# Optimization experiments

Measured on AMD Instinct MI355X. Metric: run time of the kernel, lower is better.

## Reference

```python
import jax, jax.numpy as jnp
import numpy as np

B, T, C, H, HD = 4, 2048, 1024, 16, 64

def setup_inputs() -> dict:
    key = jax.random.key(0)
    ks = jax.random.split(key, 9)
    s = 1.0 / np.sqrt(C)
    return {
        "x":  jax.random.normal(ks[0], (B, T, C), jnp.float32),
        "Wq": jax.random.normal(ks[1], (H, C, HD), jnp.float32) * s,
        "bq": jax.random.normal(ks[2], (H, HD), jnp.float32) * 0.02,
        "Wk": jax.random.normal(ks[3], (H, C, HD), jnp.float32) * s,
        "bk": jax.random.normal(ks[4], (H, HD), jnp.float32) * 0.02,
        "Wv": jax.random.normal(ks[5], (H, C, HD), jnp.float32) * s,
        "bv": jax.random.normal(ks[6], (H, HD), jnp.float32) * 0.02,
        "Wo": jax.random.normal(ks[7], (C, C), jnp.float32) * s,
        "bo": jax.random.normal(ks[8], (C,), jnp.float32) * 0.02,
    }

def reference(x, Wq, bq, Wk, bk, Wv, bv, Wo, bo):
    # Batched per-head linear projections: [B,T,C] x [H,C,D] -> [B,H,T,D]
    q = jnp.einsum('btc,hcd->bhtd', x, Wq) + bq[None, :, None, :]
    k = jnp.einsum('btc,hcd->bhtd', x, Wk) + bk[None, :, None, :]
    v = jnp.einsum('btc,hcd->bhtd', x, Wv) + bv[None, :, None, :]
    scale = 1.0 / jnp.sqrt(jnp.asarray(HD, q.dtype))
    scores = jnp.einsum('bhtd,bhsd->bhts', q, k) * scale  # [B,H,T,T]
    causal = jnp.tril(jnp.ones((T, T), dtype=bool))
    scores = jnp.where(causal[None, None, :, :], scores, -jnp.inf)
    attn = jax.nn.softmax(scores, axis=-1)
    out = jnp.einsum('bhts,bhsd->bhtd', attn, v)          # [B,H,T,D]
    concat = out.transpose(0, 2, 1, 3).reshape(B, T, C)   # concat heads
    return concat @ Wo + bo
```

## Files before the change

### kernel.cpp

```cpp
#include <hip/hip_runtime.h>
#include <stdint.h>

#define TSEQ 2048
#define NHEAD 16

typedef __attribute__((ext_vector_type(8))) short bf16x8;
typedef __attribute__((ext_vector_type(4))) short bf16x4;
typedef __attribute__((ext_vector_type(4))) float f32x4;

__device__ __forceinline__ unsigned short f2bf(float f) {
  union { float f; uint32_t u; } c;
  c.f = f;
  uint32_t u = c.u;
  u += 0x7fffu + ((u >> 16) & 1u);
  return (unsigned short)(u >> 16);
}

__device__ __forceinline__ float fexp2(float x) {
#if __has_builtin(__builtin_amdgcn_exp2f)
  return __builtin_amdgcn_exp2f(x);
#else
  return __builtin_exp2f(x);
#endif
}

using as3_void  = __attribute__((address_space(3))) void;
using as1_cvoid = const __attribute__((address_space(1))) void;

__device__ __forceinline__ void gld_lds16(const void* g, void* l) {
  __builtin_amdgcn_global_load_lds((as1_cvoid*)g, (as3_void*)l, 16, 0, 0);
}


__global__ void cast_x_kernel(const float4* __restrict__ x, unsigned short* __restrict__ xb) {
  int i = blockIdx.x * 256 + threadIdx.x;
  float4 v = x[i];
  int e = i * 4;
  int m = e >> 10, k = e & 1023;
  int ks = k ^ ((m & 7) << 3);
  ushort4 o;
  o.x = f2bf(v.x); o.y = f2bf(v.y); o.z = f2bf(v.z); o.w = f2bf(v.w);
  *(ushort4*)(xb + (size_t)m * 1024 + ks) = o;
}

__global__ void repack_wqkv(const float* __restrict__ Wq, const float* __restrict__ Wk,
                            const float* __restrict__ Wv, unsigned short* __restrict__ BT) {
  __shared__ unsigned short tile[64][72];
  const float* W = (blockIdx.z == 0) ? Wq : (blockIdx.z == 1) ? Wk : Wv;
  const int h = blockIdx.y;
  const int c0 = blockIdx.x * 64;
  const int t = threadIdx.x;
  const float* src = W + ((size_t)h * 1024 + c0) * 64;
#pragma unroll
  for (int p = 0; p < 16; ++p) {
    int idx = p * 256 + t;
    int cc = idx >> 6, d = idx & 63;
    tile[cc][d] = f2bf(src[(size_t)cc * 64 + d]);
  }
  __syncthreads();
  unsigned short* dst = BT + ((size_t)blockIdx.z * 1024 + (size_t)h * 64) * 1024 + c0;
#pragma unroll
  for (int p = 0; p < 16; ++p) {
    int idx = p * 256 + t;
    int d = idx >> 6, cc = idx & 63;
    dst[(size_t)d * 1024 + (cc ^ ((d & 7) << 3))] = tile[cc][d];
  }
}

__global__ void repack_wo(const float* __restrict__ Wo, unsigned short* __restrict__ WoT) {
  __shared__ unsigned short tile[64][72];
  const int k0 = blockIdx.x * 64;
  const int n0 = blockIdx.y * 64;
  const int t = threadIdx.x;
#pragma unroll
  for (int p = 0; p < 16; ++p) {
    int idx = p * 256 + t;
    int kk = idx >> 6, nn = idx & 63;
    tile[kk][nn] = f2bf(Wo[(size_t)(k0 + kk) * 1024 + n0 + nn]);
  }
  __syncthreads();
#pragma unroll
  for (int p = 0; p < 16; ++p) {
    int idx = p * 256 + t;
    int nn = idx >> 6, kk = idx & 63;
    WoT[(size_t)(n0 + nn) * 1024 + k0 + (kk ^ ((nn & 7) << 3))] = tile[kk][nn];
  }
}


template <int MODE>
__global__ __launch_bounds__(256) void gemm_bt(
    const unsigned short* __restrict__ A, const unsigned short* __restrict__ BTm,
    const float* __restrict__ bias0, const float* __restrict__ bias1,
    const float* __restrict__ bias2,
    unsigned short* __restrict__ qo, unsigned short* __restrict__ ko,
    unsigned short* __restrict__ vto, float* __restrict__ outf,
    int K, int N) {
  __shared__ __align__(16) char lds[65536];

  const int tid = threadIdx.x, lane = tid & 63, wv = tid >> 6;
  const int wr = wv >> 1, wc = wv & 1;
  const int g = lane >> 4, r = lane & 15;
  const int m0 = blockIdx.x * 128, n0 = blockIdx.y * 128;
  const int xr = (r & 7) << 4;

  f32x4 acc[4][4] = {};

  const int arow = tid >> 3;
  const int acol = (tid & 7) * 8;
  const unsigned short* Ab = A + (size_t)(m0 + arow) * K + acol;
  const unsigned short* Bb = BTm + (size_t)(n0 + arow) * K + acol;

#define GSTAGE(b, kel) do {                                                 \
    char* ab_ = lds + (b) * 32768 + wv * 1024;                              \
    _Pragma("unroll") for (int i = 0; i < 4; ++i) {                         \
      gld_lds16(Ab + (size_t)i * 32 * K + (kel), ab_ + i * 4096);           \
      gld_lds16(Bb + (size_t)i * 32 * K + (kel), ab_ + 16384 + i * 4096);   \
    } } while (0)

  const int NT = K >> 6;
  GSTAGE(0, 0);
  __syncthreads();

  for (int t = 0; t < NT; ++t) {
    const int cur = t & 1;
    if (t + 1 < NT) GSTAGE(cur ^ 1, (t + 1) << 6);
    const char* Ar = lds + cur * 32768;
    const char* Br = Ar + 16384;
#pragma unroll
    for (int kk = 0; kk < 2; ++kk) {
      bf16x8 af[4], bfv[4];
#pragma unroll
      for (int f = 0; f < 4; ++f) {
        af[f]  = *(const bf16x8*)(Ar + (wr * 64 + f * 16 + r) * 128 + ((kk * 64 + g * 16) ^ xr));
        bfv[f] = *(const bf16x8*)(Br + (wc * 64 + f * 16 + r) * 128 + ((kk * 64 + g * 16) ^ xr));
      }
#pragma unroll
      for (int fm = 0; fm < 4; ++fm)
#pragma unroll
        for (int fn = 0; fn < 4; ++fn)
          acc[fm][fn] = __builtin_amdgcn_mfma_f32_16x16x32_bf16(af[fm], bfv[fn], acc[fm][fn], 0, 0, 0);
    }
    __syncthreads();
  }
#undef GSTAGE

  if (MODE == 0) {
    const int which = n0 >> 10;
    const float* bias = (which == 0) ? bias0 : (which == 1) ? bias1 : bias2;
    const float sc = (which == 0) ? 0.18033688011112042f : 1.0f;
    const int b = m0 >> 11;
    const int t0 = m0 & 2047;
    unsigned short* ep = (unsigned short*)lds;

#pragma unroll
    for (int h = 0; h < 2; ++h) {
      const int head = ((n0 & 1023) + h * 64) >> 6;
      const size_t bhb = (size_t)(b * NHEAD + head) * 131072;
      __syncthreads();
      if (wc == h) {
        if (which == 2) {
#pragma unroll
          for (int fn = 0; fn < 4; ++fn) {
            const int d = fn * 16 + r;
            const float bvl = bias[head * 64 + d];
#pragma unroll
            for (int fm = 0; fm < 4; ++fm)
#pragma unroll
              for (int j = 0; j < 4; ++j) {
                const int t = wr * 64 + fm * 16 + 4 * g + j;
                ep[d * 136 + t] = f2bf(acc[fm][fn][j] + bvl);
              }
          }
        } else {
#pragma unroll
          for (int fn = 0; fn < 4; ++fn) {
            const int d = fn * 16 + r;
            const float bvl = bias[head * 64 + d];
#pragma unroll
            for (int fm = 0; fm < 4; ++fm)
#pragma unroll
              for (int j = 0; j < 4; ++j) {
                const int t = wr * 64 + fm * 16 + 4 * g + j;
                ep[t * 72 + d] = f2bf((acc[fm][fn][j] + bvl) * sc);
              }
          }
        }
      }
      __syncthreads();
      if (which == 2) {
#pragma unroll
        for (int p = 0; p < 4; ++p) {
          const int d = p * 16 + (tid >> 4);
          const int u = tid & 15;
          const int c = u >> 3;
          const int w = u & 7;
          const int kk = w >> 2, gg = w & 3;
          const int base_t = c * 64 + kk * 32 + 4 * gg;
          union { bf16x4 h4[2]; bf16x8 v8; } cc2;
          cc2.h4[0] = *(const bf16x4*)(ep + d * 136 + base_t);
          cc2.h4[1] = *(const bf16x4*)(ep + d * 136 + base_t + 16);
          const int q_base = w * 8;
          *(bf16x8*)(vto + bhb + (size_t)((t0 >> 6) + c) * 4096 + (size_t)d * 64 +
                     (q_base ^ ((d & 7) << 3))) = cc2.v8;
        }
      } else {
        unsigned short* qk = (which == 1) ? ko : qo;
#pragma unroll
        for (int p = 0; p < 4; ++p) {
          const int row = p * 32 + (tid >> 3);
          const int seg = tid & 7;
          const bf16x8 v8 = *(const bf16x8*)(ep + row * 72 + seg * 8);
          const int tt = t0 + row;
          int dbase = seg * 8;
          if (which == 1) dbase ^= (tt & 7) << 3;
          *(bf16x8*)(qk + bhb + (size_t)tt * 64 + dbase) = v8;
        }
      }
    }
  } else {
    float* epf = (float*)lds;
#pragma unroll
    for (int h = 0; h < 2; ++h) {
      __syncthreads();
      if (wc == h) {
#pragma unroll
        for (int fn = 0; fn < 4; ++fn) {
          const int n = n0 + h * 64 + fn * 16 + r;
          const float bvl = bias0[n];
#pragma unroll
          for (int fm = 0; fm < 4; ++fm)
#pragma unroll
            for (int j = 0; j < 4; ++j)
              epf[(wr * 64 + fm * 16 + 4 * g + j) * 68 + fn * 16 + r] = acc[fm][fn][j] + bvl;
        }
      }
      __syncthreads();
#pragma unroll
      for (int p = 0; p < 8; ++p) {
        const int row = p * 16 + (tid >> 4);
        const int seg = tid & 15;
        const f32x4 v4 = *(const f32x4*)(epf + row * 68 + seg * 4);
        *(f32x4*)(outf + (size_t)(m0 + row) * N + n0 + h * 64 + seg * 4) = v4;
      }
    }
  }
}


__global__ __launch_bounds__(256) void attn_fwd(const unsigned short* __restrict__ Qm,
                                                const unsigned short* __restrict__ Km,
                                                const unsigned short* __restrict__ Vtm,
                                                unsigned short* __restrict__ Om) {
  __shared__ __align__(16) unsigned short Ks[2][4096];
  __shared__ __align__(16) unsigned short Vs[2][4096];

  const int tid = threadIdx.x, lane = tid & 63, wv = tid >> 6;
  const int g = lane >> 4, r = lane & 15;
  const int bh = blockIdx.x & 63;
  const int qp = 15 - (blockIdx.x >> 6);

  const unsigned short* Qp = Qm + (size_t)bh * 131072;
  const unsigned short* Kp = Km + (size_t)bh * 131072;
  const unsigned short* Vp = Vtm + (size_t)bh * 131072;

  const int qb[2] = {qp * 128 + wv * 16, qp * 128 + 64 + wv * 16};
  const int nt = qp * 2 + 2;

  bf16x8 qf[2][2];
#pragma unroll
  for (int mi = 0; mi < 2; ++mi)
#pragma unroll
    for (int h2 = 0; h2 < 2; ++h2)
      qf[mi][h2] = *(const bf16x8*)(Qp + (size_t)(qb[mi] + r) * 64 + h2 * 32 + g * 8);

  f32x4 oacc[2][4] = {};
  float m_[2] = {-__builtin_inff(), -__builtin_inff()};
  float l_[2] = {0.f, 0.f};

  const uint32_t sw = (uint32_t)((r & 7) << 4);
  const uint32_t ob = (uint32_t)(r * 128);
  const uint32_t c0 = ((uint32_t)(g * 16)) ^ sw;
  const uint32_t c1 = ((uint32_t)(64 + g * 16)) ^ sw;
  const char* const KsB = (const char*)Ks;
  const char* const VsB = (const char*)Vs;

#define ASTAGE(buf, c) do {                                                      \
    const unsigned short* kg_ = Kp + (size_t)(c) * 4096;                         \
    const unsigned short* vg_ = Vp + (size_t)(c) * 4096;                         \
    const int o0_ = wv * 1024;                                                   \
    gld_lds16(kg_ + (o0_ >> 1) + lane * 8, (char*)Ks[buf] + o0_);                \
    gld_lds16(vg_ + (o0_ >> 1) + lane * 8, (char*)Vs[buf] + o0_);                \
    gld_lds16(kg_ + ((o0_ + 4096) >> 1) + lane * 8, (char*)Ks[buf] + o0_ + 4096);\
    gld_lds16(vg_ + ((o0_ + 4096) >> 1) + lane * 8, (char*)Vs[buf] + o0_ + 4096);\
  } while (0)

  ASTAGE(0, 0);
  __syncthreads();

  for (int t = 0; t < nt; ++t) {
    const uint32_t bo = (uint32_t)((t & 1) << 13);
    if (t + 1 < nt) ASTAGE((t & 1) ^ 1, t + 1);

    const char* pk0 = KsB + bo + ob + c0;
    const char* pk1 = KsB + bo + ob + c1;
    const char* pv0 = VsB + bo + ob + c0;
    const char* pv1 = VsB + bo + ob + c1;
    bf16x8 kf[4][2], vf[4][2];
#pragma unroll
    for (int tt = 0; tt < 4; ++tt) {
      kf[tt][0] = *(const bf16x8*)(pk0 + tt * 2048);
      kf[tt][1] = *(const bf16x8*)(pk1 + tt * 2048);
      vf[tt][0] = *(const bf16x8*)(pv0 + tt * 2048);
      vf[tt][1] = *(const bf16x8*)(pv1 + tt * 2048);
    }

#pragma unroll
    for (int mi = 0; mi < 2; ++mi) {
      const int qbm = qb[mi];
      if (t * 64 > qbm + 15) continue;

      f32x4 sT[4];
      __builtin_amdgcn_s_setprio(1);
#pragma unroll
      for (int tt = 0; tt < 4; ++tt) {
        f32x4 a = {0.f, 0.f, 0.f, 0.f};
        a = __builtin_amdgcn_mfma_f32_16x16x32_bf16(kf[tt][0], qf[mi][0], a, 0, 0, 0);
        a = __builtin_amdgcn_mfma_f32_16x16x32_bf16(kf[tt][1], qf[mi][1], a, 0, 0, 0);
        sT[tt] = a;
      }
      __builtin_amdgcn_s_setprio(0);

      const int qg = qbm + r;
      if (t * 64 + 63 > qbm) {
#pragma unroll
        for (int tt = 0; tt < 4; ++tt)
#pragma unroll
          for (int j = 0; j < 4; ++j) {
            const int kv = t * 64 + tt * 16 + 4 * g + j;
            sT[tt][j] = (kv <= qg) ? sT[tt][j] : -__builtin_inff();
          }
      }

      float tm[4];
#pragma unroll
      for (int tt = 0; tt < 4; ++tt)
        tm[tt] = fmaxf(fmaxf(sT[tt][0], sT[tt][1]), fmaxf(sT[tt][2], sT[tt][3]));
      const float mx = fmaxf(fmaxf(tm[0], tm[1]), fmaxf(tm[2], tm[3]));

      float mcur = m_[mi];
      const bool norescale = __all(mx <= mcur + 4.0f);
      if (!norescale) {
        float rmx = mx;
        rmx = fmaxf(rmx, __shfl_xor(rmx, 16));
        rmx = fmaxf(rmx, __shfl_xor(rmx, 32));
        const float mnew = fmaxf(mcur, rmx);
        const float rs = fexp2(mcur - mnew);
        m_[mi] = mnew;
        mcur = mnew;
        l_[mi] *= rs;
        float rsb[4];
#pragma unroll
        for (int j = 0; j < 4; ++j) rsb[j] = __shfl(rs, 4 * g + j);
#pragma unroll
        for (int df = 0; df < 4; ++df)
#pragma unroll
          for (int j = 0; j < 4; ++j) oacc[mi][df][j] *= rsb[j];
      }

      float ts = 0.f;
#pragma unroll
      for (int tt = 0; tt < 4; ++tt)
#pragma unroll
        for (int j = 0; j < 4; ++j) {
          const float p = fexp2(sT[tt][j] - mcur);
          sT[tt][j] = p;
          ts += p;
        }
      l_[mi] += ts;

      union { uint32_t w[8]; bf16x8 v[2]; } pu;
#pragma unroll
      for (int tt = 0; tt < 4; ++tt) {
        asm("v_cvt_pk_bf16_f32 %0, %1, %2" : "=v"(pu.w[2 * tt])
            : "v"(sT[tt][0]), "v"(sT[tt][1]));
        asm("v_cvt_pk_bf16_f32 %0, %1, %2" : "=v"(pu.w[2 * tt + 1])
            : "v"(sT[tt][2]), "v"(sT[tt][3]));
      }

      __builtin_amdgcn_s_setprio(1);
#pragma unroll
      for (int kk = 0; kk < 2; ++kk)
#pragma unroll
        for (int df = 0; df < 4; ++df)
          oacc[mi][df] = __builtin_amdgcn_mfma_f32_16x16x32_bf16(pu.v[kk], vf[df][kk], oacc[mi][df], 0, 0, 0);
      __builtin_amdgcn_s_setprio(0);
    }
    __syncthreads();
  }
#undef ASTAGE

  const int b = bh >> 4, h = bh & 15;
#pragma unroll
  for (int mi = 0; mi < 2; ++mi) {
    float lt = l_[mi];
    lt += __shfl_xor(lt, 16);
    lt += __shfl_xor(lt, 32);
    float inv[4];
#pragma unroll
    for (int j = 0; j < 4; ++j) {
      const float lb = __shfl(lt, 4 * g + j);
      inv[j] = __builtin_amdgcn_rcpf(lb);
    }
#pragma unroll
    for (int df = 0; df < 4; ++df)
#pragma unroll
      for (int j = 0; j < 4; ++j) {
        const int trow = qb[mi] + 4 * g + j;
        const float ov = oacc[mi][df][j] * inv[j];
        const int col = (df * 16 + r) ^ ((trow & 7) << 3);
        Om[((size_t)(b * TSEQ + trow)) * 1024 + h * 64 + col] = f2bf(ov);
      }
  }
}


extern "C" void kernel_launch(void* const* d_in, const int* in_sizes, int n_in,
                              void* d_out, int out_size, void* d_ws, size_t ws_size,
                              hipStream_t stream) {
  const float* x  = (const float*)d_in[0];
  const float* Wq = (const float*)d_in[1];
  const float* bq = (const float*)d_in[2];
  const float* Wk = (const float*)d_in[3];
  const float* bk = (const float*)d_in[4];
  const float* Wv = (const float*)d_in[5];
  const float* bv = (const float*)d_in[6];
  const float* Wo = (const float*)d_in[7];
  const float* bo = (const float*)d_in[8];
  float* out = (float*)d_out;

  unsigned short* xb  = (unsigned short*)d_ws;
  unsigned short* btq = xb + (size_t)8192 * 1024;
  unsigned short* wot = btq + (size_t)3072 * 1024;
  unsigned short* qb  = wot + (size_t)1024 * 1024;
  unsigned short* kb  = qb + (size_t)64 * 2048 * 64;
  unsigned short* vtb = kb + (size_t)64 * 2048 * 64;

  cast_x_kernel<<<8192, 256, 0, stream>>>((const float4*)x, xb);
  repack_wqkv<<<dim3(16, 16, 3), 256, 0, stream>>>(Wq, Wk, Wv, btq);
  repack_wo<<<dim3(16, 16), 256, 0, stream>>>(Wo, wot);

  gemm_bt<0><<<dim3(64, 24), 256, 0, stream>>>(xb, btq, bq, bk, bv, qb, kb, vtb,
                                               nullptr, 1024, 3072);
  attn_fwd<<<1024, 256, 0, stream>>>(qb, kb, vtb, xb);
  gemm_bt<1><<<dim3(64, 8), 256, 0, stream>>>(xb, wot, bo, nullptr, nullptr,
                                              nullptr, nullptr, nullptr, out,
                                              1024, 1024);
}
```

Before: 178.1 us.

## Halve attention query tile to 64 rows and double block count

Each attention block now handles 64 query rows instead of 128, with one 16-row tile per wave, and the grid doubles to 2048 blocks. This raises parallelism and occupancy, since fewer registers are needed for accumulators, and makes the causal workload more balanced across blocks. In exchange, every K/V tile loaded into LDS is reused by half as many query rows, so global and LDS traffic for K/V roughly doubles.

```diff
diff --git a/kernel.cpp b/kernel.cpp
--- a/kernel.cpp
+++ b/kernel.cpp
@@ -258,25 +258,23 @@
   const int tid = threadIdx.x, lane = tid & 63, wv = tid >> 6;
   const int g = lane >> 4, r = lane & 15;
   const int bh = blockIdx.x & 63;
-  const int qp = 15 - (blockIdx.x >> 6);
+  const int p = 31 - (blockIdx.x >> 6);
+  const int nt = p + 1;
 
   const unsigned short* Qp = Qm + (size_t)bh * 131072;
   const unsigned short* Kp = Km + (size_t)bh * 131072;
   const unsigned short* Vp = Vtm + (size_t)bh * 131072;
 
-  const int qb[2] = {qp * 128 + wv * 16, qp * 128 + 64 + wv * 16};
-  const int nt = qp * 2 + 2;
-
-  bf16x8 qf[2][2];
-#pragma unroll
-  for (int mi = 0; mi < 2; ++mi)
-#pragma unroll
-    for (int h2 = 0; h2 < 2; ++h2)
-      qf[mi][h2] = *(const bf16x8*)(Qp + (size_t)(qb[mi] + r) * 64 + h2 * 32 + g * 8);
-
-  f32x4 oacc[2][4] = {};
-  float m_[2] = {-__builtin_inff(), -__builtin_inff()};
-  float l_[2] = {0.f, 0.f};
+  const int qb = p * 64 + wv * 16;
+
+  bf16x8 qf[2];
+#pragma unroll
+  for (int h2 = 0; h2 < 2; ++h2)
+    qf[h2] = *(const bf16x8*)(Qp + (size_t)(qb + r) * 64 + h2 * 32 + g * 8);
+
+  f32x4 oacc[4] = {};
+  float m_ = -__builtin_inff();
+  float l_ = 0.f;
 
   const uint32_t sw = (uint32_t)((r & 7) << 4);
   const uint32_t ob = (uint32_t)(r * 128);
@@ -315,113 +313,105 @@
       vf[tt][1] = *(const bf16x8*)(pv1 + tt * 2048);
     }
 
-#pragma unroll
-    for (int mi = 0; mi < 2; ++mi) {
-      const int qbm = qb[mi];
-      if (t * 64 > qbm + 15) continue;
-
-      f32x4 sT[4];
-      __builtin_amdgcn_s_setprio(1);
-#pragma unroll
-      for (int tt = 0; tt < 4; ++tt) {
-        f32x4 a = {0.f, 0.f, 0.f, 0.f};
-        a = __builtin_amdgcn_mfma_f32_16x16x32_bf16(kf[tt][0], qf[mi][0], a, 0, 0, 0);
-        a = __builtin_amdgcn_mfma_f32_16x16x32_bf16(kf[tt][1], qf[mi][1], a, 0, 0, 0);
-        sT[tt] = a;
-      }
-      __builtin_amdgcn_s_setprio(0);
-
-      const int qg = qbm + r;
-      if (t * 64 + 63 > qbm) {
-#pragma unroll
-        for (int tt = 0; tt < 4; ++tt)
-#pragma unroll
-          for (int j = 0; j < 4; ++j) {
-            const int kv = t * 64 + tt * 16 + 4 * g + j;
-            sT[tt][j] = (kv <= qg) ? sT[tt][j] : -__builtin_inff();
-          }
-      }
-
-      float tm[4];
+    f32x4 sT[4];
+    __builtin_amdgcn_s_setprio(1);
+#pragma unroll
+    for (int tt = 0; tt < 4; ++tt) {
+      f32x4 a = {0.f, 0.f, 0.f, 0.f};
+      a = __builtin_amdgcn_mfma_f32_16x16x32_bf16(kf[tt][0], qf[0], a, 0, 0, 0);
+      a = __builtin_amdgcn_mfma_f32_16x16x32_bf16(kf[tt][1], qf[1], a, 0, 0, 0);
+      sT[tt] = a;
+    }
+    __builtin_amdgcn_s_setprio(0);
+
+    const int qg = qb + r;
+    if (t * 64 + 63 > qb) {
 #pragma unroll
       for (int tt = 0; tt < 4; ++tt)
-        tm[tt] = fmaxf(fmaxf(sT[tt][0], sT[tt][1]), fmaxf(sT[tt][2], sT[tt][3]));
-      const float mx = fmaxf(fmaxf(tm[0], tm[1]), fmaxf(tm[2], tm[3]));
-
-      float mcur = m_[mi];
-      const bool norescale = __all(mx <= mcur + 4.0f);
-      if (!norescale) {
-        float rmx = mx;
-        rmx = fmaxf(rmx, __shfl_xor(rmx, 16));
-        rmx = fmaxf(rmx, __shfl_xor(rmx, 32));
-        const float mnew = fmaxf(mcur, rmx);
-        const float rs = fexp2(mcur - mnew);
-        m_[mi] = mnew;
-        mcur = mnew;
-        l_[mi] *= rs;
-        float rsb[4];
-#pragma unroll
-        for (int j = 0; j < 4; ++j) rsb[j] = __shfl(rs, 4 * g + j);
-#pragma unroll
-        for (int df = 0; df < 4; ++df)
-#pragma unroll
-          for (int j = 0; j < 4; ++j) oacc[mi][df][j] *= rsb[j];
-      }
-
-      float ts = 0.f;
-#pragma unroll
-      for (int tt = 0; tt < 4; ++tt)
 #pragma unroll
         for (int j = 0; j < 4; ++j) {
-          const float p = fexp2(sT[tt][j] - mcur);
-          sT[tt][j] = p;
-          ts += p;
+          const int kv = t * 64 + tt * 16 + 4 * g + j;
+          sT[tt][j] = (kv <= qg) ? sT[tt][j] : -__builtin_inff();
         }
-      l_[mi] += ts;
-
-      union { uint32_t w[8]; bf16x8 v[2]; } pu;
-#pragma unroll
-      for (int tt = 0; tt < 4; ++tt) {
-        asm("v_cvt_pk_bf16_f32 %0, %1, %2" : "=v"(pu.w[2 * tt])
-            : "v"(sT[tt][0]), "v"(sT[tt][1]));
-        asm("v_cvt_pk_bf16_f32 %0, %1, %2" : "=v"(pu.w[2 * tt + 1])
-            : "v"(sT[tt][2]), "v"(sT[tt][3]));
-      }
-
-      __builtin_amdgcn_s_setprio(1);
-#pragma unroll
-      for (int kk = 0; kk < 2; ++kk)
-#pragma unroll
-        for (int df = 0; df < 4; ++df)
-          oacc[mi][df] = __builtin_amdgcn_mfma_f32_16x16x32_bf16(pu.v[kk], vf[df][kk], oacc[mi][df], 0, 0, 0);
-      __builtin_amdgcn_s_setprio(0);
-    }
+    }
+
+    float tm[4];
+#pragma unroll
+    for (int tt = 0; tt < 4; ++tt)
+      tm[tt] = fmaxf(fmaxf(sT[tt][0], sT[tt][1]), fmaxf(sT[tt][2], sT[tt][3]));
+    const float mx = fmaxf(fmaxf(tm[0], tm[1]), fmaxf(tm[2], tm[3]));
+
+    float mcur = m_;
+    const bool norescale = __all(mx <= mcur + 4.0f);
+    if (!norescale) {
+      float rmx = mx;
+      rmx = fmaxf(rmx, __shfl_xor(rmx, 16));
+      rmx = fmaxf(rmx, __shfl_xor(rmx, 32));
+      const float mnew = fmaxf(mcur, rmx);
+      const float rs = fexp2(mcur - mnew);
+      m_ = mnew;
+      mcur = mnew;
+      l_ *= rs;
+      float rsb[4];
+#pragma unroll
+      for (int j = 0; j < 4; ++j) rsb[j] = __shfl(rs, 4 * g + j);
+#pragma unroll
+      for (int df = 0; df < 4; ++df)
+#pragma unroll
+        for (int j = 0; j < 4; ++j) oacc[df][j] *= rsb[j];
+    }
+
+    float ts = 0.f;
+#pragma unroll
+    for (int tt = 0; tt < 4; ++tt)
+#pragma unroll
+      for (int j = 0; j < 4; ++j) {
+        const float pp = fexp2(sT[tt][j] - mcur);
+        sT[tt][j] = pp;
+        ts += pp;
+      }
+    l_ += ts;
+
+    union { uint32_t w[8]; bf16x8 v[2]; } pu;
+#pragma unroll
+    for (int tt = 0; tt < 4; ++tt) {
+      asm("v_cvt_pk_bf16_f32 %0, %1, %2" : "=v"(pu.w[2 * tt])
+          : "v"(sT[tt][0]), "v"(sT[tt][1]));
+      asm("v_cvt_pk_bf16_f32 %0, %1, %2" : "=v"(pu.w[2 * tt + 1])
+          : "v"(sT[tt][2]), "v"(sT[tt][3]));
+    }
+
+    __builtin_amdgcn_s_setprio(1);
+#pragma unroll
+    for (int kk = 0; kk < 2; ++kk)
+#pragma unroll
+      for (int df = 0; df < 4; ++df)
+        oacc[df] = __builtin_amdgcn_mfma_f32_16x16x32_bf16(pu.v[kk], vf[df][kk], oacc[df], 0, 0, 0);
+    __builtin_amdgcn_s_setprio(0);
+
     __syncthreads();
   }
 #undef ASTAGE
 
   const int b = bh >> 4, h = bh & 15;
-#pragma unroll
-  for (int mi = 0; mi < 2; ++mi) {
-    float lt = l_[mi];
-    lt += __shfl_xor(lt, 16);
-    lt += __shfl_xor(lt, 32);
-    float inv[4];
+  float lt = l_;
+  lt += __shfl_xor(lt, 16);
+  lt += __shfl_xor(lt, 32);
+  float inv[4];
+#pragma unroll
+  for (int j = 0; j < 4; ++j) {
+    const float lb = __shfl(lt, 4 * g + j);
+    inv[j] = __builtin_amdgcn_rcpf(lb);
+  }
+#pragma unroll
+  for (int df = 0; df < 4; ++df)
 #pragma unroll
     for (int j = 0; j < 4; ++j) {
-      const float lb = __shfl(lt, 4 * g + j);
-      inv[j] = __builtin_amdgcn_rcpf(lb);
-    }
-#pragma unroll
-    for (int df = 0; df < 4; ++df)
-#pragma unroll
-      for (int j = 0; j < 4; ++j) {
-        const int trow = qb[mi] + 4 * g + j;
-        const float ov = oacc[mi][df][j] * inv[j];
-        const int col = (df * 16 + r) ^ ((trow & 7) << 3);
-        Om[((size_t)(b * TSEQ + trow)) * 1024 + h * 64 + col] = f2bf(ov);
-      }
-  }
+      const int trow = qb + 4 * g + j;
+      const float ov = oacc[df][j] * inv[j];
+      const int col = (df * 16 + r) ^ ((trow & 7) << 3);
+      Om[((size_t)(b * TSEQ + trow)) * 1024 + h * 64 + col] = f2bf(ov);
+    }
 }
 
 
@@ -452,7 +442,7 @@
 
   gemm_bt<0><<<dim3(64, 24), 256, 0, stream>>>(xb, btq, bq, bk, bv, qb, kb, vtb,
                                                nullptr, 1024, 3072);
-  attn_fwd<<<1024, 256, 0, stream>>>(qb, kb, vtb, xb);
+  attn_fwd<<<2048, 256, 0, stream>>>(qb, kb, vtb, xb);
   gemm_bt<1><<<dim3(64, 8), 256, 0, stream>>>(xb, wot, bo, nullptr, nullptr,
                                               nullptr, nullptr, nullptr, out,
                                               1024, 1024);
```

New measurement: 178.1 us. About the same (+0.0%).
